# Performance work log

Measured on AMD Instinct MI355X. Metric: run time of the kernel, lower is better.

Reference implementation:

```python
import jax, jax.numpy as jnp
import numpy as np

NUM_LEVELS = 4
RADIUS = 4
H, W = 64, 128


def _bilinear_sample(feat, x, y):
    # feat: [N, Hl, Wl]; x, y: [N, K, K] pixel coords; zeros padding, align_corners=True
    N, Hl, Wl = feat.shape
    x0 = jnp.floor(x)
    y0 = jnp.floor(y)
    x1 = x0 + 1.0
    y1 = y0 + 1.0
    wx1 = x - x0
    wx0 = 1.0 - wx1
    wy1 = y - y0
    wy0 = 1.0 - wy1
    n_idx = jnp.arange(N)[:, None, None]

    def gather(xi, yi):
        inb = (xi >= 0) & (xi <= Wl - 1) & (yi >= 0) & (yi <= Hl - 1)
        xc = jnp.clip(xi, 0, Wl - 1).astype(jnp.int32)
        yc = jnp.clip(yi, 0, Hl - 1).astype(jnp.int32)
        v = feat[n_idx, yc, xc]
        return jnp.where(inb, v, jnp.zeros((), feat.dtype))

    return (gather(x0, y0) * wx0 * wy0 + gather(x1, y0) * wx1 * wy0
            + gather(x0, y1) * wx0 * wy1 + gather(x1, y1) * wx1 * wy1)


def _correlation(fmap1, fmap2, coords):
    bs, dim, h, w = fmap1.shape
    f1 = fmap1.reshape(bs, dim, h * w)
    f2 = fmap2.reshape(bs, dim, h * w)
    cv = jnp.einsum('bdm,bdn->bmn', f1, f2) / jnp.sqrt(jnp.asarray(dim, jnp.float32))
    cv = cv.reshape(bs * h * w, h, w)
    pyramid = [cv]
    for _ in range(NUM_LEVELS - 1):
        N, hl, wl = cv.shape
        cv = cv.reshape(N, hl // 2, 2, wl // 2, 2).mean(axis=(2, 4))  # avg_pool2d(2,2)
        pyramid.append(cv)

    cxy = coords.transpose(0, 2, 3, 1).astype(jnp.float32)  # [bs,h,w,2]
    cx = cxy[..., 0].reshape(-1)  # [bs*h*w]
    cy = cxy[..., 1].reshape(-1)
    r = RADIUS
    d = jnp.linspace(-r, r, 2 * r + 1, dtype=jnp.float32)
    dy, dx = jnp.meshgrid(d, d, indexing='ij')  # [K,K]

    outs = []
    for i, corr in enumerate(pyramid):
        scale = jnp.float32(2 ** i)
        x = cx[:, None, None] / scale + dx[None]
        y = cy[:, None, None] / scale + dy[None]
        sampled = _bilinear_sample(corr, x, y)  # [bs*h*w, K, K]
        outs.append(sampled.reshape(bs, h, w, -1))
    out = jnp.concatenate(outs, axis=-1)  # [bs,h,w,num_levels*K*K]
    return out.transpose(0, 3, 1, 2)


def setup_inputs() -> dict:
    key = jax.random.key(0)
    k1, k2, k3, k4 = jax.random.split(key, 4)
    fmap1 = jax.random.normal(k1, (1, 256, H, W), dtype=jnp.float32)
    fmap2 = jax.random.normal(k2, (1, 256, H, W), dtype=jnp.float32)
    cx = jax.random.uniform(k3, (1, 1, H, W), dtype=jnp.float32) * (W - 1)
    cy = jax.random.uniform(k4, (1, 1, H, W), dtype=jnp.float32) * (H - 1)
    coords = jnp.concatenate([cx, cy], axis=1)  # [1,2,H,W], channel 0 = x, 1 = y
    return {"fmap1": fmap1, "fmap2": fmap2, "coords": coords}


def reference(fmap1, fmap2, coords):
    return _correlation(fmap1, fmap2, coords)
```

## Files before the change

### kernel.cpp

```cpp
#include <hip/hip_runtime.h>
#include <stdint.h>

typedef _Float16 f16;
typedef __attribute__((ext_vector_type(8))) _Float16 f16x8;
typedef __attribute__((ext_vector_type(4))) float f32x4;
typedef __attribute__((ext_vector_type(2))) float fv2;
typedef __attribute__((ext_vector_type(4))) float fv4;

#define H0 64
#define W0 128
#define NPIX 8192
#define KD 256
#define NCAT 10880
#define OFF1 8192
#define OFF2 10240
#define OFF3 10752
#define CAP0 640
#define CAP1 2048
#define PL1OFF (32 * CAP0)
#define PLTOT (PL1OFF + 8 * CAP1)
#define ZTOT (64 + PLTOT + 64)


__global__ __launch_bounds__(256) void fused_pre(const float* __restrict__ in0,
                                                 const float* __restrict__ in1,
                                                 f16* __restrict__ At,
                                                 f16* __restrict__ Bt,
                                                 int* __restrict__ cnt) {
  __shared__ f16 tile[64][65];
  int bid = blockIdx.x;
  int t = threadIdx.x;

  if (bid < 1024) {
    const float* in = (bid < 512) ? in0 : in1;
    f16* out = (bid < 512) ? At : Bt;
    size_t NR = (bid < 512) ? NPIX : NCAT;
    int bx = bid & 511;
    int m0 = (bx & 127) * 64;
    int d0 = (bx >> 7) * 64;
    int a = t & 63, b = t >> 6;
#pragma unroll
    for (int i = 0; i < 16; ++i) {
      int d = b + i * 4;
      tile[a][d] = (f16)in[(size_t)(d0 + d) * NPIX + m0 + a];
    }
    __syncthreads();
#pragma unroll
    for (int i = 0; i < 16; ++i) {
      int m = b + i * 4;
      int d = d0 + a;
      out[((size_t)(d >> 5) * NR + (m0 + m)) * 32 + (d & 31)] = tile[m][a];
    }
  } else if (bid < 1360) {
    int idx = (bid - 1024) * 256 + t;
    float acc[8] = {0, 0, 0, 0, 0, 0, 0, 0};
    int r, dc;
    if (idx < 65536) {
      int r1 = idx & 2047; dc = idx >> 11; r = r1;
      int y = r1 >> 6, x = r1 & 63;
#pragma unroll
      for (int e = 0; e < 8; ++e) {
        const float* p = in1 + (size_t)(dc * 8 + e) * NPIX + (y * 2) * W0 + x * 2;
        fv2 s0 = *(const fv2*)p;
        fv2 s1 = *(const fv2*)(p + W0);
        acc[e] = (s0[0] + s0[1] + s1[0] + s1[1]) * 0.25f;
      }
    } else if (idx < 81920) {
      int i2 = idx - 65536;
      int r2 = i2 & 511; dc = i2 >> 9; r = 2048 + r2;
      int y = r2 >> 5, x = r2 & 31;
#pragma unroll
      for (int e = 0; e < 8; ++e) {
        const float* p = in1 + (size_t)(dc * 8 + e) * NPIX + (y * 4) * W0 + x * 4;
        float s = 0.f;
#pragma unroll
        for (int h = 0; h < 4; ++h) {
          fv4 v = *(const fv4*)(p + h * W0);
          s += v[0] + v[1] + v[2] + v[3];
        }
        acc[e] = s * 0.0625f;
      }
    } else {
      int i3 = idx - 81920;
      int r3 = i3 & 127; dc = i3 >> 7; r = 2560 + r3;
      int y = r3 >> 4, x = r3 & 15;
#pragma unroll
      for (int e = 0; e < 8; ++e) {
        const float* p = in1 + (size_t)(dc * 8 + e) * NPIX + (y * 8) * W0 + x * 8;
        float s = 0.f;
#pragma unroll
        for (int h = 0; h < 8; ++h) {
          fv4 v0 = *(const fv4*)(p + h * W0);
          fv4 v1 = *(const fv4*)(p + h * W0 + 4);
          s += v0[0] + v0[1] + v0[2] + v0[3] + v1[0] + v1[1] + v1[2] + v1[3];
        }
        acc[e] = s * 0.015625f;
      }
    }
    f16x8 o;
#pragma unroll
    for (int e = 0; e < 8; ++e) o[e] = (f16)acc[e];
    *(f16x8*)(Bt + ((size_t)(dc >> 2) * NCAT + 8192 + r) * 32 + (dc & 3) * 8) = o;
  } else {
    int idx = (bid - 1360) * 256 + t;
    if (idx < ZTOT) cnt[idx] = 0;
  }
}

__global__ __launch_bounds__(1024) void bucket_build(const float* __restrict__ coords,
                                                     int2* __restrict__ meta,
                                                     int* __restrict__ cnt) {
  __shared__ int hist[40];
  __shared__ int base[40];
  int* plist = cnt + 64;
  int t = threadIdx.x;
  int m = blockIdx.x * 1024 + t;
  if (t < 40) hist[t] = 0;
  __syncthreads();

  float cx = coords[m];
  float cy = coords[NPIX + m];
  int X0l[2], Y0l[2];
  int mx = 0, my = 0;
#pragma unroll
  for (int lev = 0; lev < 4; ++lev) {
    float inv = 1.0f / (float)(1 << lev);
    int X0 = (int)floorf(cx * inv) - 4;
    int Y0 = (int)floorf(cy * inv) - 4;
    if (lev < 2) { X0l[lev] = X0; Y0l[lev] = Y0; }
    mx |= (X0 & 0xff) << (8 * lev);
    my |= (Y0 & 0xff) << (8 * lev);
  }
  meta[m] = make_int2(mx, my);

  int b0 = (min(max(Y0l[0], 0), 63) >> 4) * 8 + (min(max(X0l[0], 0), 127) >> 4);
  int b1 = (min(max(Y0l[1], 0), 31) >> 4) * 4 + (min(max(X0l[1], 0), 63) >> 4);
  int s0 = atomicAdd(&hist[b0], 1);
  int s1 = atomicAdd(&hist[32 + b1], 1);
  __syncthreads();

  if (t < 40) base[t] = atomicAdd(&cnt[t], hist[t]);
  __syncthreads();

  int p0 = base[b0] + s0;
  if (p0 < CAP0) plist[b0 * CAP0 + p0] = m;
  int p1 = base[32 + b1] + s1;
  if (p1 < CAP1) plist[PL1OFF + b1 * CAP1 + p1] = m;
}

__global__ __launch_bounds__(256, 2) void gemm_all(const f16* __restrict__ At,
                                                   const f16* __restrict__ Bt,
                                                   const int* __restrict__ cnt,
                                                   const int2* __restrict__ meta,
                                                   f16* __restrict__ Wbuf) {
  __shared__ f16 sa[8192];
  const int* plist = cnt + 64;
  int bid = blockIdx.x;
  int t = threadIdx.x;
  int lane = t & 63;
  int w = t >> 6;
  int lr = lane & 15;
  int ko = lane >> 4;

  if (bid < 160) {
    int bm = (((bid & 7) << 2) | ((bid >> 3) & 3)) << 8;
    int bn = OFF2 + ((bid >> 5) << 7);

    const f16* Ab = At + (size_t)(bm + w * 64 + lr) * 32 + ko * 8;
    const f16* Bb = Bt + (size_t)(bn + lr) * 32 + ko * 8;

    f16x8 af[2][4], bf[2][8];
#define LOADK(s, kk)                                                           \
    do {                                                                       \
      const f16* ap = Ab + (size_t)(kk) * (NPIX * 32);                         \
      const f16* bp = Bb + (size_t)(kk) * (NCAT * 32);                         \
      _Pragma("unroll")                                                        \
      for (int i = 0; i < 4; ++i) af[s][i] = *(const f16x8*)(ap + i * 512);    \
      _Pragma("unroll")                                                        \
      for (int i = 0; i < 8; ++i) bf[s][i] = *(const f16x8*)(bp + i * 512);    \
    } while (0)

    f32x4 acc[4][8];
#pragma unroll
    for (int i = 0; i < 4; ++i)
#pragma unroll
      for (int j = 0; j < 8; ++j) acc[i][j] = (f32x4){0.f, 0.f, 0.f, 0.f};

    LOADK(0, 0);
    LOADK(1, 1);
#pragma unroll
    for (int kk = 0; kk < 8; ++kk) {
      const int cur = kk & 1;
#pragma unroll
      for (int mi = 0; mi < 4; ++mi)
#pragma unroll
        for (int ni = 0; ni < 8; ++ni)
          acc[mi][ni] = __builtin_amdgcn_mfma_f32_16x16x32_f16(
              af[cur][mi], bf[cur][ni], acc[mi][ni], 0, 0, 0);
      if (kk + 2 < 8) LOADK(cur, kk + 2);
    }
#undef LOADK

    int lev, n0, wlog;
    if (bn < OFF3) { lev = 2; n0 = bn - OFF2; wlog = 5; }
    else           { lev = 3; n0 = bn - OFF3; wlog = 4; }
    int wmask = (1 << wlog) - 1;
    int yA = n0 >> wlog;
    int yB = (n0 + 127) >> wlog;
    int ycol[8], xcol[8];
#pragma unroll
    for (int ni = 0; ni < 8; ++ni) {
      int n = n0 + ni * 16 + lr;
      ycol[ni] = n >> wlog;
      xcol[ni] = n & wmask;
    }
    int sh = lev * 8;
#pragma unroll
    for (int mi = 0; mi < 4; ++mi)
#pragma unroll
      for (int r2 = 0; r2 < 4; ++r2) {
        int grow = bm + w * 64 + mi * 16 + ko * 4 + r2;
        int2 mv = meta[grow];
        int Y0 = (int)(signed char)((mv.y >> sh) & 0xff);
        if (Y0 <= yB && Y0 + 9 >= yA) {
          int X0 = (int)(signed char)((mv.x >> sh) & 0xff);
          f16* rowp = Wbuf + (size_t)grow * 512 + lev * 128;
#pragma unroll
          for (int ni = 0; ni < 8; ++ni) {
            int dy = ycol[ni] - Y0;
            int dx = xcol[ni] - X0;
            if ((unsigned)dy < 10u && (unsigned)dx < 10u)
              rowp[dy * 12 + dx] = (f16)(acc[mi][ni][r2] * 0.0625f);
          }
        }
      }
    return;
  }

  int bb = bid - 160;
  int xcd = bb & 7;
  int s = bb >> 3;
  int lev, b, mg, half;
  if (s < 160) { lev = 0; int j = s / 40; int r = s - j * 40; b = xcd * 4 + j; mg = r >> 1; half = r & 1; }
  else         { lev = 1; int r = s - 160; b = xcd; mg = r >> 1; half = r & 1; }

  int CAP   = lev ? CAP1 : CAP0;
  int cb    = min(cnt[lev ? 32 + b : b], CAP);
  if (mg * 32 >= cb) return;
  int Hl    = lev ? 32 : 64;
  int Wmap  = lev ? 64 : 128;
  int bx    = lev ? (b & 3) : (b & 7);
  int by    = lev ? (b >> 2) : (b >> 3);
  int x0 = bx * 16, y0 = by * 16;
  int NY = min(25, Hl - y0);
  int rowbase = lev ? 8192 : 0;
  int pbase = (lev ? PL1OFF + b * CAP1 : b * CAP0) + mg * 32;

  {
    int spix = t >> 3;
    int skk  = t & 7;
    int sp = plist[pbase + spix] & (NPIX - 1);
    const f16* g = At + (size_t)skk * (NPIX * 32) + (size_t)sp * 32;
    int line = spix >> 1;
    int sb = (spix & 1) * 4;
    f16* dst = sa + skk * 1024 + line * 64;
#pragma unroll
    for (int q = 0; q < 4; ++q) {
      int phys = (sb + q) ^ (line & 7) ^ skk;
      *(f16x8*)(dst + phys * 8) = *(const f16x8*)(g + q * 8);
    }
  }

  int aoff[2];
#pragma unroll
  for (int mi = 0; mi < 2; ++mi) {
    int pl = mi * 16 + lr;
    int line = pl >> 1;
    int phys = ((pl & 1) * 4 + ko) ^ (line & 7);
    aoff[mi] = line * 64 + phys * 8;
  }

  bool vst[4];
  int brow[4];
#pragma unroll
  for (int st = 0; st < 4; ++st) {
    int q = w + 4 * st;
    int yl = half * 13 + q;
    vst[st] = (q < (half ? 12 : 13)) && (yl < NY);
    int ylc = min(yl, NY - 1);
    brow[st] = rowbase + (y0 + ylc) * Wmap + x0 + lr;
  }

  f16x8 bf[3][8];
#define BLDB(s_, kk_)                                                          \
  do {                                                                         \
    const f16* bp = Bt + (size_t)(kk_) * (NCAT * 32) + ko * 8;                 \
    _Pragma("unroll")                                                          \
    for (int st = 0; st < 4; ++st) {                                           \
      bf[s_][st * 2]     = *(const f16x8*)(bp + (size_t)brow[st] * 32);        \
      bf[s_][st * 2 + 1] = *(const f16x8*)(bp + (size_t)(brow[st] + 16) * 32); \
    }                                                                          \
  } while (0)

  BLDB(0, 0);
  BLDB(1, 1);
  BLDB(2, 2);

  f32x4 acc[8][2];
#pragma unroll
  for (int i = 0; i < 8; ++i)
#pragma unroll
    for (int j = 0; j < 2; ++j) acc[i][j] = (f32x4){0.f, 0.f, 0.f, 0.f};

  __syncthreads();

#pragma unroll
  for (int kk = 0; kk < 8; ++kk) {
    const int cur = kk % 3;
    f16x8 a0 = *(const f16x8*)(sa + kk * 1024 + (aoff[0] ^ (kk * 8)));
    f16x8 a1 = *(const f16x8*)(sa + kk * 1024 + (aoff[1] ^ (kk * 8)));
#pragma unroll
    for (int nf = 0; nf < 8; ++nf) {
      acc[nf][0] = __builtin_amdgcn_mfma_f32_16x16x32_f16(a0, bf[cur][nf],
                                                          acc[nf][0], 0, 0, 0);
      acc[nf][1] = __builtin_amdgcn_mfma_f32_16x16x32_f16(a1, bf[cur][nf],
                                                          acc[nf][1], 0, 0, 0);
    }
    if (kk + 3 < 8) BLDB(cur, kk + 3);
  }
#undef BLDB

  int pe[2][4];
  int Xp[2][4], Yp[2][4];
  int sh = lev * 8;
#pragma unroll
  for (int mi = 0; mi < 2; ++mi)
#pragma unroll
    for (int r2 = 0; r2 < 4; ++r2) {
      int slot = mg * 32 + mi * 16 + ko * 4 + r2;
      int p = plist[pbase + mi * 16 + ko * 4 + r2] & (NPIX - 1);
      pe[mi][r2] = (slot < cb) ? p : -1;
      int2 mv = meta[p];
      Xp[mi][r2] = (int)(signed char)((mv.x >> sh) & 0xff);
      Yp[mi][r2] = (int)(signed char)((mv.y >> sh) & 0xff);
    }
#pragma unroll
  for (int st = 0; st < 4; ++st) {
    if (!vst[st]) continue;
    int y = y0 + half * 13 + w + 4 * st;
#pragma unroll
    for (int xc = 0; xc < 2; ++xc) {
      int x = x0 + xc * 16 + lr;
#pragma unroll
      for (int mi = 0; mi < 2; ++mi)
#pragma unroll
        for (int r2 = 0; r2 < 4; ++r2) {
          int p = pe[mi][r2];
          int dy = y - Yp[mi][r2];
          int dx = x - Xp[mi][r2];
          if (p >= 0 && (unsigned)dy < 10u && (unsigned)dx < 10u)
            Wbuf[(size_t)p * 512 + lev * 128 + dy * 12 + dx] =
                (f16)(acc[st * 2 + xc][mi][r2] * 0.0625f);
        }
    }
  }
}

__global__ __launch_bounds__(256) void corr_sample(const f16* __restrict__ Wbuf,
                                                   const float* __restrict__ coords,
                                                   float* __restrict__ out) {
  int tid = blockIdx.x * 256 + threadIdx.x;
  int m = tid & (NPIX - 1);
  int lev = tid >> 13;
  int Hl = H0 >> lev, Wl = W0 >> lev;

  float cx = coords[m];
  float cy = coords[NPIX + m];
  float inv = 1.0f / (float)(1 << lev);
  float xb = cx * inv, yb = cy * inv;
  float fx = floorf(xb), fy = floorf(yb);
  int X0 = (int)fx - 4, Y0 = (int)fy - 4;
  float wx1 = xb - fx, wx0 = 1.0f - wx1;
  float wy1 = yb - fy, wy0 = 1.0f - wy1;

  const f16* wb = Wbuf + (size_t)m * 512 + lev * 128;
  f16x8 rv[15];
#pragma unroll
  for (int i = 0; i < 15; ++i) rv[i] = *(const f16x8*)(wb + i * 8);

  float* op = out + (size_t)lev * 81 * NPIX + m;
  float cur[11], nxt[11];
#pragma unroll
  for (int i = 0; i < 11; ++i) {
    bool in = ((unsigned)Y0 < (unsigned)Hl) && ((unsigned)(X0 + i) < (unsigned)Wl);
    cur[i] = in ? (float)rv[i >> 3][i & 7] : 0.0f;
  }
#pragma unroll
  for (int j = 0; j < 9; ++j) {
    bool yin = (unsigned)(Y0 + j + 1) < (unsigned)Hl;
#pragma unroll
    for (int i = 0; i < 11; ++i) {
      int c = (j + 1) * 12 + i;
      bool in = yin && ((unsigned)(X0 + i) < (unsigned)Wl);
      nxt[i] = in ? (float)rv[c >> 3][c & 7] : 0.0f;
    }
#pragma unroll
    for (int i = 0; i < 9; ++i) {
      float v = wy0 * (wx0 * cur[i] + wx1 * cur[i + 1])
              + wy1 * (wx0 * nxt[i] + wx1 * nxt[i + 1]);
      op[(size_t)(j * 9 + i) * NPIX] = v;
    }
#pragma unroll
    for (int i = 0; i < 11; ++i) cur[i] = nxt[i];
  }
}

extern "C" void kernel_launch(void* const* d_in, const int* in_sizes, int n_in,
                              void* d_out, int out_size, void* d_ws, size_t ws_size,
                              hipStream_t stream) {
  const float* fmap1  = (const float*)d_in[0];
  const float* fmap2  = (const float*)d_in[1];
  const float* coords = (const float*)d_in[2];
  float* out = (float*)d_out;

  char* ws = (char*)d_ws;
  size_t offA = 0;
  size_t offB = offA + (size_t)NPIX * KD * 2;
  size_t offW = offB + (size_t)NCAT * KD * 2;
  size_t offM = offW + (size_t)NPIX * 512 * 2;
  size_t offC = offM + (size_t)NPIX * 8;
  size_t need = offC + (size_t)ZTOT * 4;
  if (ws_size < need) return;

  f16*  At   = (f16*)(ws + offA);
  f16*  Bt   = (f16*)(ws + offB);
  f16*  Wbuf = (f16*)(ws + offW);
  int2* meta = (int2*)(ws + offM);
  int*  cnt  = (int*)(ws + offC);

  fused_pre<<<1505, 256, 0, stream>>>(fmap1, fmap2, At, Bt, cnt);
  bucket_build<<<8, 1024, 0, stream>>>(coords, meta, cnt);
  gemm_all<<<2464, 256, 0, stream>>>(At, Bt, cnt, meta, Wbuf);
  corr_sample<<<128, 256, 0, stream>>>(Wbuf, coords, out);
}
```

Measured before the change: 76.05 us.

## Retile sparse-level GEMM blocks to 64 pixels by quarter row-slab

The sparse level-0/1 correlation blocks now handle 64 gathered pixels (up to 7 map rows, a quarter slab) instead of 32 pixels and half the rows. The A tile in shared memory doubles, each wave keeps 4x4 MFMA accumulators, and B is double-buffered instead of triple-buffered. The aim is more reuse of each B fragment across pixels and less redundant B traffic. The trade-offs are that fewer blocks do useful work for sparse bins, the LDS footprint grows, and prefetch depth drops.

```diff
diff --git a/kernel.cpp b/kernel.cpp
--- a/kernel.cpp
+++ b/kernel.cpp
@@ -153,7 +153,7 @@
                                                    const int* __restrict__ cnt,
                                                    const int2* __restrict__ meta,
                                                    f16* __restrict__ Wbuf) {
-  __shared__ f16 sa[8192];
+  __shared__ f16 sa[16384];
   const int* plist = cnt + 64;
   int bid = blockIdx.x;
   int t = threadIdx.x;
@@ -240,63 +240,68 @@
   int bb = bid - 160;
   int xcd = bb & 7;
   int s = bb >> 3;
-  int lev, b, mg, half;
-  if (s < 160) { lev = 0; int j = s / 40; int r = s - j * 40; b = xcd * 4 + j; mg = r >> 1; half = r & 1; }
-  else         { lev = 1; int r = s - 160; b = xcd; mg = r >> 1; half = r & 1; }
+  int lev, b, mg, q4;
+  if (s < 160) { lev = 0; int j = s / 40; int r = s - j * 40; b = xcd * 4 + j; mg = r >> 2; q4 = r & 3; }
+  else         { lev = 1; int r = s - 160; b = xcd; mg = r >> 2; q4 = r & 3; }
 
   int CAP   = lev ? CAP1 : CAP0;
   int cb    = min(cnt[lev ? 32 + b : b], CAP);
-  if (mg * 32 >= cb) return;
+  if (mg * 64 >= cb) return;
   int Hl    = lev ? 32 : 64;
   int Wmap  = lev ? 64 : 128;
   int bx    = lev ? (b & 3) : (b & 7);
   int by    = lev ? (b >> 2) : (b >> 3);
   int x0 = bx * 16, y0 = by * 16;
   int NY = min(25, Hl - y0);
+  int ys = q4 * 6;
   int rowbase = lev ? 8192 : 0;
-  int pbase = (lev ? PL1OFF + b * CAP1 : b * CAP0) + mg * 32;
+  int pbase = (lev ? PL1OFF + b * CAP1 : b * CAP0) + mg * 64;
 
   {
-    int spix = t >> 3;
-    int skk  = t & 7;
+    int spix = t >> 2;
+    int kp = (t & 3) * 2;
     int sp = plist[pbase + spix] & (NPIX - 1);
-    const f16* g = At + (size_t)skk * (NPIX * 32) + (size_t)sp * 32;
     int line = spix >> 1;
     int sb = (spix & 1) * 4;
-    f16* dst = sa + skk * 1024 + line * 64;
-#pragma unroll
-    for (int q = 0; q < 4; ++q) {
-      int phys = (sb + q) ^ (line & 7) ^ skk;
-      *(f16x8*)(dst + phys * 8) = *(const f16x8*)(g + q * 8);
-    }
-  }
-
-  int aoff[2];
-#pragma unroll
-  for (int mi = 0; mi < 2; ++mi) {
+#pragma unroll
+    for (int j = 0; j < 2; ++j) {
+      int skk = kp + j;
+      const f16* g = At + (size_t)skk * (NPIX * 32) + (size_t)sp * 32;
+      f16* dst = sa + skk * 2048 + line * 64;
+#pragma unroll
+      for (int q = 0; q < 4; ++q) {
+        int phys = (sb + q) ^ (line & 7) ^ skk;
+        *(f16x8*)(dst + phys * 8) = *(const f16x8*)(g + q * 8);
+      }
+    }
+  }
+
+  int aoff[4];
+#pragma unroll
+  for (int mi = 0; mi < 4; ++mi) {
     int pl = mi * 16 + lr;
     int line = pl >> 1;
     int phys = ((pl & 1) * 4 + ko) ^ (line & 7);
     aoff[mi] = line * 64 + phys * 8;
   }
 
-  bool vst[4];
-  int brow[4];
-#pragma unroll
-  for (int st = 0; st < 4; ++st) {
+  bool vst[2];
+  int brow[2];
+#pragma unroll
+  for (int st = 0; st < 2; ++st) {
     int q = w + 4 * st;
-    int yl = half * 13 + q;
-    vst[st] = (q < (half ? 12 : 13)) && (yl < NY);
+    int yl = ys + q;
+    vst[st] = (q < 7) && (yl < NY);
     int ylc = min(yl, NY - 1);
     brow[st] = rowbase + (y0 + ylc) * Wmap + x0 + lr;
   }
 
-  f16x8 bf[3][8];
+  f16x8 bf[2][4];
 #define BLDB(s_, kk_)                                                          \
   do {                                                                         \
     const f16* bp = Bt + (size_t)(kk_) * (NCAT * 32) + ko * 8;                 \
     _Pragma("unroll")                                                          \
-    for (int st = 0; st < 4; ++st) {                                           \
+    for (int st = 0; st < 2; ++st) {                                           \
       bf[s_][st * 2]     = *(const f16x8*)(bp + (size_t)brow[st] * 32);        \
       bf[s_][st * 2 + 1] = *(const f16x8*)(bp + (size_t)(brow[st] + 16) * 32); \
     }                                                                          \
@@ -304,64 +309,59 @@
 
   BLDB(0, 0);
   BLDB(1, 1);
-  BLDB(2, 2);
-
-  f32x4 acc[8][2];
-#pragma unroll
-  for (int i = 0; i < 8; ++i)
-#pragma unroll
-    for (int j = 0; j < 2; ++j) acc[i][j] = (f32x4){0.f, 0.f, 0.f, 0.f};
+
+  f32x4 acc[4][4];
+#pragma unroll
+  for (int i = 0; i < 4; ++i)
+#pragma unroll
+    for (int j = 0; j < 4; ++j) acc[i][j] = (f32x4){0.f, 0.f, 0.f, 0.f};
 
   __syncthreads();
 
 #pragma unroll
   for (int kk = 0; kk < 8; ++kk) {
-    const int cur = kk % 3;
-    f16x8 a0 = *(const f16x8*)(sa + kk * 1024 + (aoff[0] ^ (kk * 8)));
-    f16x8 a1 = *(const f16x8*)(sa + kk * 1024 + (aoff[1] ^ (kk * 8)));
-#pragma unroll
-    for (int nf = 0; nf < 8; ++nf) {
-      acc[nf][0] = __builtin_amdgcn_mfma_f32_16x16x32_f16(a0, bf[cur][nf],
-                                                          acc[nf][0], 0, 0, 0);
-      acc[nf][1] = __builtin_amdgcn_mfma_f32_16x16x32_f16(a1, bf[cur][nf],
-                                                          acc[nf][1], 0, 0, 0);
-    }
-    if (kk + 3 < 8) BLDB(cur, kk + 3);
+    const int cur = kk & 1;
+    f16x8 a[4];
+#pragma unroll
+    for (int mi = 0; mi < 4; ++mi)
+      a[mi] = *(const f16x8*)(sa + kk * 2048 + (aoff[mi] ^ (kk * 8)));
+#pragma unroll
+    for (int nf = 0; nf < 4; ++nf)
+#pragma unroll
+      for (int mi = 0; mi < 4; ++mi)
+        acc[nf][mi] = __builtin_amdgcn_mfma_f32_16x16x32_f16(
+            a[mi], bf[cur][nf], acc[nf][mi], 0, 0, 0);
+    if (kk + 2 < 8) BLDB(cur, kk + 2);
   }
 #undef BLDB
 
-  int pe[2][4];
-  int Xp[2][4], Yp[2][4];
   int sh = lev * 8;
 #pragma unroll
-  for (int mi = 0; mi < 2; ++mi)
+  for (int mi = 0; mi < 4; ++mi) {
 #pragma unroll
     for (int r2 = 0; r2 < 4; ++r2) {
-      int slot = mg * 32 + mi * 16 + ko * 4 + r2;
-      int p = plist[pbase + mi * 16 + ko * 4 + r2] & (NPIX - 1);
-      pe[mi][r2] = (slot < cb) ? p : -1;
+      int slot = mi * 16 + ko * 4 + r2;
+      int p = plist[pbase + slot] & (NPIX - 1);
+      bool pv = (mg * 64 + slot) < cb;
       int2 mv = meta[p];
-      Xp[mi][r2] = (int)(signed char)((mv.x >> sh) & 0xff);
-      Yp[mi][r2] = (int)(signed char)((mv.y >> sh) & 0xff);
-    }
-#pragma unroll
-  for (int st = 0; st < 4; ++st) {
-    if (!vst[st]) continue;
-    int y = y0 + half * 13 + w + 4 * st;
-#pragma unroll
-    for (int xc = 0; xc < 2; ++xc) {
-      int x = x0 + xc * 16 + lr;
-#pragma unroll
-      for (int mi = 0; mi < 2; ++mi)
-#pragma unroll
-        for (int r2 = 0; r2 < 4; ++r2) {
-          int p = pe[mi][r2];
-          int dy = y - Yp[mi][r2];
-          int dx = x - Xp[mi][r2];
-          if (p >= 0 && (unsigned)dy < 10u && (unsigned)dx < 10u)
-            Wbuf[(size_t)p * 512 + lev * 128 + dy * 12 + dx] =
-                (f16)(acc[st * 2 + xc][mi][r2] * 0.0625f);
+      int X0 = (int)(signed char)((mv.x >> sh) & 0xff);
+      int Y0 = (int)(signed char)((mv.y >> sh) & 0xff);
+#pragma unroll
+      for (int st = 0; st < 2; ++st) {
+        if (!vst[st]) continue;
+        int y = y0 + ys + w + 4 * st;
+        int dy = y - Y0;
+        if (pv && (unsigned)dy < 10u) {
+#pragma unroll
+          for (int xc = 0; xc < 2; ++xc) {
+            int x = x0 + xc * 16 + lr;
+            int dx = x - X0;
+            if ((unsigned)dx < 10u)
+              Wbuf[(size_t)p * 512 + lev * 128 + dy * 12 + dx] =
+                  (f16)(acc[st * 2 + xc][mi][r2] * 0.0625f);
+          }
         }
+      }
     }
   }
 }
```

Result: slower. 80.99 us (+6.5%).
